# Kernel optimization log

Hardware: AMD Instinct MI355X
Metric: run time of the kernel (lower is better)

The kernel has to match this reference:

```python
import jax, jax.numpy as jnp
import numpy as np

PSIZE = 3
PSTRIDE = 3
N = PSIZE * PSTRIDE   # 9 attention tokens
P = PSIZE ** 2        # 9 pixels per token


def setup_inputs() -> dict:
    key = jax.random.key(0)
    k1, k2, k3, k4, k5 = jax.random.split(key, 5)
    B, H, W, C = 8192, 9, 9, 256
    hidden = C // 2
    x = jax.random.normal(k1, (B, H, W, C), dtype=jnp.float32)
    W_fc = jax.random.normal(k2, (hidden, C), dtype=jnp.float32) * (C ** -0.5)
    b_fc = jax.random.normal(k3, (hidden,), dtype=jnp.float32) * 0.01
    block_idx = jax.random.randint(k4, (B,), 0, 1024, dtype=jnp.int32)
    match_vec = jax.random.randint(k5, (1024, 1), 0, 2, dtype=jnp.int32)
    return {"x": x, "W_fc": W_fc, "b_fc": b_fc, "block_idx": block_idx, "match_vec": match_vec}


def reference(x, W_fc, b_fc, block_idx, match_vec):
    B, H, Wd, C = x.shape
    hidden = W_fc.shape[0]
    scale = (hidden * P) ** -0.5

    # [B, pstride, psize, pstride, psize, C] -> patch-major [B, ps, ps, p, p, C]
    xv = x.reshape(B, PSTRIDE, PSIZE, PSTRIDE, PSIZE, C).transpose(0, 1, 3, 2, 4, 5)
    x_fc = xv.reshape(B, N, P, C)

    # linear projection C -> hidden, then flatten pixels: q [B, N, P*hidden]
    q = (jnp.einsum('bnpc,hc->bnph', x_fc, W_fc) + b_fc).reshape(B, N, P * hidden)

    attn = jnp.einsum('bnd,bmd->bnm', q, q) * scale  # [B, N, N]

    # additive mask: -100 on diagonal, zeroed out entirely for matched samples
    base = jnp.where(jnp.eye(N, dtype=bool), jnp.float32(-100.0), jnp.float32(0.0))
    cur_match = match_vec[block_idx].squeeze(-1)  # [B]
    mask = jnp.where(cur_match[:, None, None] == 1, jnp.float32(0.0), base[None])

    attn = jax.nn.softmax(attn + mask, axis=-1)

    v = xv.reshape(B, N, P * C)
    out = attn @ v  # [B, N, P*C]

    out = out.reshape(B, PSTRIDE, PSTRIDE, PSIZE, PSIZE, C)
    out = out.transpose(0, 1, 3, 2, 4, 5).reshape(B, H, Wd, C)
    return out
```

## Files before the change

kernel.cpp:

```cpp
#include <hip/hip_runtime.h>

typedef short short8 __attribute__((ext_vector_type(8)));
typedef float floatx16 __attribute__((ext_vector_type(16)));
typedef float floatx4 __attribute__((ext_vector_type(4)));

#define ROWS 81
#define CDIM 256
#define XT   0
#define QT   41472
#define SC   66048
#define AB   70144
#define TOT  70656

#define SWX(r) ((((r) & 15) << 4) ^ (((r) & 8) << 3))

__device__ __forceinline__ unsigned short f2bf(float f) {
    union { float f; unsigned int u; } v; v.f = f;
    return (unsigned short)((v.u + 0x7FFFu + ((v.u >> 16) & 1u)) >> 16);
}

__device__ __forceinline__ unsigned int cvtpk(float lo, float hi) {
    unsigned int r;
    asm("v_cvt_pk_bf16_f32 %0, %1, %2" : "=v"(r) : "v"(lo), "v"(hi));
    return r;
}

__global__ void wconv_kernel(const float* __restrict__ W,
                             unsigned short* __restrict__ Wb, int n) {
    int i = blockIdx.x * 256 + threadIdx.x;
    if (i < n) Wb[i] = f2bf(W[i]);
}

__device__ __forceinline__ void stage_store(char* smem, int k, float4 a0, float4 a1) {
    int gr = k >> 5;
    int c0 = (k & 31) * 8;
    int hh = gr / 9, ww = gr - hh * 9;
    int p = (hh % 3) * 3 + (ww % 3);
    int m = (hh / 3) * 3 + (ww / 3);
    int r = p * 9 + m;
    uint4 v;
    v.x = cvtpk(a0.x, a0.y);
    v.y = cvtpk(a0.z, a0.w);
    v.z = cvtpk(a1.x, a1.y);
    v.w = cvtpk(a1.z, a1.w);
    *(uint4*)(smem + XT + r * 512 + ((c0 * 2) ^ SWX(r))) = v;
}

__global__ __launch_bounds__(512, 2)
void attn_kernel(const float* __restrict__ x,
                 const unsigned short* __restrict__ Wb,
                 const float* __restrict__ b_fc,
                 const int* __restrict__ block_idx,
                 const int* __restrict__ match_vec,
                 float* __restrict__ out)
{
    __shared__ __align__(16) char smem[TOT];
    const int b     = blockIdx.x;
    const int t     = threadIdx.x;
    const int lane  = t & 63;
    const int wave  = t >> 6;
    const int l15   = lane & 15;
    const int kg    = lane >> 4;
    const int l31   = lane & 31;
    const int khalf = lane >> 5;

    int cm = 0;
    if (t < 9) cm = match_vec[block_idx[b]];

    const int rh = (wave & 1) * 48;
    const int hg = (wave >> 1) * 32;

    short8 wfrag[2][8];
#pragma unroll
    for (int s2 = 0; s2 < 2; ++s2) {
        const unsigned short* wr = Wb + (hg + s2 * 16 + l15) * CDIM + kg * 8;
#pragma unroll
        for (int ks = 0; ks < 8; ++ks)
            wfrag[s2][ks] = *(const short8*)(wr + ks * 32);
    }
    float bias2[2];
    bias2[0] = b_fc[hg + l15];
    bias2[1] = b_fc[hg + 16 + l15];

    {
        const float* xb = x + (size_t)b * (ROWS * CDIM);
        float4 a0[5], a1[5], t0, t1;
#pragma unroll
        for (int j = 0; j < 5; ++j) {
            int k = t + 512 * j;
            a0[j] = *(const float4*)(xb + k * 8);
            a1[j] = *(const float4*)(xb + k * 8 + 4);
        }
        const bool tail = (t < 32);
        if (tail) {
            t0 = *(const float4*)(xb + (2560 + t) * 8);
            t1 = *(const float4*)(xb + (2560 + t) * 8 + 4);
        }
#pragma unroll
        for (int j = 0; j < 5; ++j) stage_store(smem, t + 512 * j, a0[j], a1[j]);
        if (tail) stage_store(smem, 2560 + t, t0, t1);
    }
    __syncthreads();

    {
        floatx4 acc[3][2];
#pragma unroll
        for (int ii = 0; ii < 3; ++ii)
#pragma unroll
            for (int s2 = 0; s2 < 2; ++s2)
#pragma unroll
                for (int j = 0; j < 4; ++j) acc[ii][s2][j] = 0.f;
#pragma unroll
        for (int ks = 0; ks < 8; ++ks) {
            int cb = ks * 64 + kg * 16;
#pragma unroll
            for (int tile = 0; tile < 3; ++tile) {
                int r = rh + tile * 16 + l15;
                short8 a = *(const short8*)(smem + XT + r * 512 + (cb ^ SWX(r)));
                acc[tile][0] = __builtin_amdgcn_mfma_f32_16x16x32_bf16(a, wfrag[0][ks], acc[tile][0], 0, 0, 0);
                acc[tile][1] = __builtin_amdgcn_mfma_f32_16x16x32_bf16(a, wfrag[1][ks], acc[tile][1], 0, 0, 0);
            }
        }
#pragma unroll
        for (int tile = 0; tile < 3; ++tile)
#pragma unroll
            for (int s2 = 0; s2 < 2; ++s2) {
                int h2 = (hg + s2 * 16 + l15) * 2;
#pragma unroll
                for (int reg = 0; reg < 4; ++reg) {
                    int r = rh + tile * 16 + kg * 4 + reg;
                    *(unsigned short*)(smem + QT + r * 256 + (h2 ^ ((r & 15) << 4))) =
                        f2bf(acc[tile][s2][reg] + bias2[s2]);
                }
            }
    }
    __syncthreads();

    if (wave < 4) {
        floatx4 g;
#pragma unroll
        for (int ii = 0; ii < 4; ++ii) g[ii] = 0.f;
        int nc = (l15 < 9) ? l15 : 8;
#pragma unroll
        for (int s = 0; s < 9; ++s) {
            int ks = wave + s * 4;
            int kk = ks * 32 + kg * 8;
            int p  = kk >> 7;
            int h0 = (kk & 127) * 2;
            int row = p * 9 + nc;
            short8 f = *(const short8*)(smem + QT + row * 256 + (h0 ^ ((row & 15) << 4)));
            g = __builtin_amdgcn_mfma_f32_16x16x32_bf16(f, f, g, 0, 0, 0);
        }
        float* sc = (float*)(smem + SC + wave * 1024);
#pragma unroll
        for (int reg = 0; reg < 4; ++reg)
            sc[(kg * 4 + reg) * 16 + l15] = g[reg];
    }
    __syncthreads();

    if (t < 9) {
        const float scale = 0.029462782549439483f;
        const float* sc0 = (const float*)(smem + SC);
        const float* sc1 = (const float*)(smem + SC + 1024);
        const float* sc2 = (const float*)(smem + SC + 2048);
        const float* sc3 = (const float*)(smem + SC + 3072);
        float s[9];
        float mx = -1e30f;
#pragma unroll
        for (int m = 0; m < 9; ++m) {
            int o = t * 16 + m;
            float v = (sc0[o] + sc1[o] + sc2[o] + sc3[o]) * scale;
            if (m == t && cm != 1) v -= 100.f;
            s[m] = v;
            mx = fmaxf(mx, v);
        }
        float sum = 0.f;
#pragma unroll
        for (int m = 0; m < 9; ++m) { s[m] = __expf(s[m] - mx); sum += s[m]; }
        float inv = 1.f / sum;
        unsigned short* ab = (unsigned short*)(smem + AB) + t * 16;
#pragma unroll
        for (int m = 0; m < 9; ++m) ab[m] = f2bf(s[m] * inv);
#pragma unroll
        for (int m = 9; m < 16; ++m) ab[m] = 0;
    }
    __syncthreads();

    {
        const int n  = l31;
        const int nm = (n < 9) ? n : 0;
        short8 bf = *(const short8*)(smem + AB + nm * 32 + khalf * 16);
        floatx16 zero16;
#pragma unroll
        for (int ii = 0; ii < 16; ++ii) zero16[ii] = 0.f;
        float* ob = out + (size_t)b * (ROWS * CDIM);
        int hh = 0, ww = 0;
        if (n < 9) { hh = (n / 3) * 3; ww = (n % 3) * 3; }
#pragma unroll
        for (int tt = 0; tt < 9; ++tt) {
            int tile = wave * 9 + tt;
            int p = tile >> 3;
            int c = (tile & 7) * 32 + l31;
            short8 af;
#pragma unroll
            for (int j = 0; j < 8; ++j) {
                int mm = khalf * 8 + j; if (mm > 8) mm = 8;
                int row = p * 9 + mm;
                af[j] = *(const short*)(smem + XT + row * 512 + ((c * 2) ^ SWX(row)));
            }
            floatx16 dacc = __builtin_amdgcn_mfma_f32_32x32x16_bf16(af, bf, zero16, 0, 0, 0);
            if (n < 9) {
#pragma unroll
                for (int q2 = 0; q2 < 4; ++q2) {
                    int c0 = (tile & 7) * 32 + q2 * 8 + khalf * 4;
                    int gr = (hh + p / 3) * 9 + (ww + p % 3);
                    *(float4*)(ob + gr * CDIM + c0) =
                        make_float4(dacc[q2 * 4 + 0], dacc[q2 * 4 + 1],
                                    dacc[q2 * 4 + 2], dacc[q2 * 4 + 3]);
                }
            }
        }
    }
}

extern "C" void kernel_launch(void* const* d_in, const int* in_sizes, int n_in,
                              void* d_out, int out_size, void* d_ws, size_t ws_size,
                              hipStream_t stream) {
    const float* x    = (const float*)d_in[0];
    const float* W    = (const float*)d_in[1];
    const float* bfc  = (const float*)d_in[2];
    const int*   bidx = (const int*)d_in[3];
    const int*   mvec = (const int*)d_in[4];
    float* outp = (float*)d_out;
    unsigned short* Wb = (unsigned short*)d_ws;

    int nW = in_sizes[1];
    wconv_kernel<<<(nW + 255) / 256, 256, 0, stream>>>(W, Wb, nW);

    int B = in_sizes[0] / (ROWS * CDIM);
    attn_kernel<<<B, 512, 0, stream>>>(x, Wb, bfc, bidx, mvec, outp);
}
```

Before: 345.5 us.

## Make attention kernel persistent with double-buffered prefetch of next batch's input

The kernel becomes persistent: a grid of at most 256 blocks each loops over a contiguous chunk of batch elements. The x tile is double-buffered in shared memory. Wave 0 computes the Gram matrix and the softmax alone, while the other seven waves load and convert the next batch element into the spare buffer. This hides global load latency behind compute and removes a barrier and the cross-wave score reduction, but raises LDS use to about 109KB per block, which limits occupancy to one block per CU. Only 256 blocks may also underfill the device's CUs.

```diff
diff --git a/kernel.cpp b/kernel.cpp
--- a/kernel.cpp
+++ b/kernel.cpp
@@ -6,11 +6,11 @@
 
 #define ROWS 81
 #define CDIM 256
-#define XT   0
-#define QT   41472
-#define SC   66048
-#define AB   70144
-#define TOT  70656
+#define XSZ  41472
+#define QT   82944
+#define SC   107520
+#define AB   108544
+#define TOT  109056
 
 #define SWX(r) ((((r) & 15) << 4) ^ (((r) & 8) << 3))
 
@@ -31,7 +31,7 @@
     if (i < n) Wb[i] = f2bf(W[i]);
 }
 
-__device__ __forceinline__ void stage_store(char* smem, int k, float4 a0, float4 a1) {
+__device__ __forceinline__ void stage_store(char* xbuf, int k, float4 a0, float4 a1) {
     int gr = k >> 5;
     int c0 = (k & 31) * 8;
     int hh = gr / 9, ww = gr - hh * 9;
@@ -43,7 +43,7 @@
     v.y = cvtpk(a0.z, a0.w);
     v.z = cvtpk(a1.x, a1.y);
     v.w = cvtpk(a1.z, a1.w);
-    *(uint4*)(smem + XT + r * 512 + ((c0 * 2) ^ SWX(r))) = v;
+    *(uint4*)(xbuf + r * 512 + ((c0 * 2) ^ SWX(r))) = v;
 }
 
 __global__ __launch_bounds__(512, 2)
@@ -52,10 +52,10 @@
                  const float* __restrict__ b_fc,
                  const int* __restrict__ block_idx,
                  const int* __restrict__ match_vec,
-                 float* __restrict__ out)
+                 float* __restrict__ out,
+                 int B, int nIter)
 {
     __shared__ __align__(16) char smem[TOT];
-    const int b     = blockIdx.x;
     const int t     = threadIdx.x;
     const int lane  = t & 63;
     const int wave  = t >> 6;
@@ -63,9 +63,8 @@
     const int kg    = lane >> 4;
     const int l31   = lane & 31;
     const int khalf = lane >> 5;
-
-    int cm = 0;
-    if (t < 9) cm = match_vec[block_idx[b]];
+    const int base  = blockIdx.x * nIter;
+    if (base >= B) return;
 
     const int rh = (wave & 1) * 48;
     const int hg = (wave >> 1) * 32;
@@ -83,7 +82,7 @@
     bias2[1] = b_fc[hg + 16 + l15];
 
     {
-        const float* xb = x + (size_t)b * (ROWS * CDIM);
+        const float* xb = x + (size_t)base * (ROWS * CDIM);
         float4 a0[5], a1[5], t0, t1;
 #pragma unroll
         for (int j = 0; j < 5; ++j) {
@@ -102,121 +101,147 @@
     }
     __syncthreads();
 
-    {
-        floatx4 acc[3][2];
-#pragma unroll
-        for (int ii = 0; ii < 3; ++ii)
-#pragma unroll
-            for (int s2 = 0; s2 < 2; ++s2)
-#pragma unroll
-                for (int j = 0; j < 4; ++j) acc[ii][s2][j] = 0.f;
-#pragma unroll
-        for (int ks = 0; ks < 8; ++ks) {
-            int cb = ks * 64 + kg * 16;
-#pragma unroll
-            for (int tile = 0; tile < 3; ++tile) {
-                int r = rh + tile * 16 + l15;
-                short8 a = *(const short8*)(smem + XT + r * 512 + (cb ^ SWX(r)));
-                acc[tile][0] = __builtin_amdgcn_mfma_f32_16x16x32_bf16(a, wfrag[0][ks], acc[tile][0], 0, 0, 0);
-                acc[tile][1] = __builtin_amdgcn_mfma_f32_16x16x32_bf16(a, wfrag[1][ks], acc[tile][1], 0, 0, 0);
-            }
-        }
-#pragma unroll
-        for (int tile = 0; tile < 3; ++tile)
-#pragma unroll
-            for (int s2 = 0; s2 < 2; ++s2) {
-                int h2 = (hg + s2 * 16 + l15) * 2;
-#pragma unroll
-                for (int reg = 0; reg < 4; ++reg) {
-                    int r = rh + tile * 16 + kg * 4 + reg;
-                    *(unsigned short*)(smem + QT + r * 256 + (h2 ^ ((r & 15) << 4))) =
-                        f2bf(acc[tile][s2][reg] + bias2[s2]);
-                }
-            }
-    }
-    __syncthreads();
-
-    if (wave < 4) {
-        floatx4 g;
-#pragma unroll
-        for (int ii = 0; ii < 4; ++ii) g[ii] = 0.f;
-        int nc = (l15 < 9) ? l15 : 8;
-#pragma unroll
-        for (int s = 0; s < 9; ++s) {
-            int ks = wave + s * 4;
-            int kk = ks * 32 + kg * 8;
-            int p  = kk >> 7;
-            int h0 = (kk & 127) * 2;
-            int row = p * 9 + nc;
-            short8 f = *(const short8*)(smem + QT + row * 256 + (h0 ^ ((row & 15) << 4)));
-            g = __builtin_amdgcn_mfma_f32_16x16x32_bf16(f, f, g, 0, 0, 0);
-        }
-        float* sc = (float*)(smem + SC + wave * 1024);
-#pragma unroll
-        for (int reg = 0; reg < 4; ++reg)
-            sc[(kg * 4 + reg) * 16 + l15] = g[reg];
-    }
-    __syncthreads();
-
-    if (t < 9) {
-        const float scale = 0.029462782549439483f;
-        const float* sc0 = (const float*)(smem + SC);
-        const float* sc1 = (const float*)(smem + SC + 1024);
-        const float* sc2 = (const float*)(smem + SC + 2048);
-        const float* sc3 = (const float*)(smem + SC + 3072);
-        float s[9];
-        float mx = -1e30f;
-#pragma unroll
-        for (int m = 0; m < 9; ++m) {
-            int o = t * 16 + m;
-            float v = (sc0[o] + sc1[o] + sc2[o] + sc3[o]) * scale;
-            if (m == t && cm != 1) v -= 100.f;
-            s[m] = v;
-            mx = fmaxf(mx, v);
-        }
-        float sum = 0.f;
-#pragma unroll
-        for (int m = 0; m < 9; ++m) { s[m] = __expf(s[m] - mx); sum += s[m]; }
-        float inv = 1.f / sum;
-        unsigned short* ab = (unsigned short*)(smem + AB) + t * 16;
-#pragma unroll
-        for (int m = 0; m < 9; ++m) ab[m] = f2bf(s[m] * inv);
-#pragma unroll
-        for (int m = 9; m < 16; ++m) ab[m] = 0;
-    }
-    __syncthreads();
-
-    {
-        const int n  = l31;
-        const int nm = (n < 9) ? n : 0;
-        short8 bf = *(const short8*)(smem + AB + nm * 32 + khalf * 16);
-        floatx16 zero16;
-#pragma unroll
-        for (int ii = 0; ii < 16; ++ii) zero16[ii] = 0.f;
-        float* ob = out + (size_t)b * (ROWS * CDIM);
-        int hh = 0, ww = 0;
-        if (n < 9) { hh = (n / 3) * 3; ww = (n % 3) * 3; }
-#pragma unroll
-        for (int tt = 0; tt < 9; ++tt) {
-            int tile = wave * 9 + tt;
-            int p = tile >> 3;
-            int c = (tile & 7) * 32 + l31;
-            short8 af;
-#pragma unroll
-            for (int j = 0; j < 8; ++j) {
-                int mm = khalf * 8 + j; if (mm > 8) mm = 8;
-                int row = p * 9 + mm;
-                af[j] = *(const short*)(smem + XT + row * 512 + ((c * 2) ^ SWX(row)));
-            }
-            floatx16 dacc = __builtin_amdgcn_mfma_f32_32x32x16_bf16(af, bf, zero16, 0, 0, 0);
-            if (n < 9) {
-#pragma unroll
-                for (int q2 = 0; q2 < 4; ++q2) {
-                    int c0 = (tile & 7) * 32 + q2 * 8 + khalf * 4;
-                    int gr = (hh + p / 3) * 9 + (ww + p % 3);
-                    *(float4*)(ob + gr * CDIM + c0) =
-                        make_float4(dacc[q2 * 4 + 0], dacc[q2 * 4 + 1],
-                                    dacc[q2 * 4 + 2], dacc[q2 * 4 + 3]);
+    for (int it = 0; it < nIter && base + it < B; ++it) {
+        const int b = base + it;
+        char* xc = smem + (it & 1) * XSZ;
+        char* xn = smem + ((it & 1) ^ 1) * XSZ;
+        const bool hasNext = (it + 1 < nIter) && (b + 1 < B);
+
+        int cm = 0;
+        if (t < 9) cm = match_vec[block_idx[b]];
+
+        {
+            floatx4 acc[3][2];
+#pragma unroll
+            for (int ii = 0; ii < 3; ++ii)
+#pragma unroll
+                for (int s2 = 0; s2 < 2; ++s2)
+#pragma unroll
+                    for (int j = 0; j < 4; ++j) acc[ii][s2][j] = 0.f;
+#pragma unroll
+            for (int ks = 0; ks < 8; ++ks) {
+                int cb = ks * 64 + kg * 16;
+#pragma unroll
+                for (int tile = 0; tile < 3; ++tile) {
+                    int r = rh + tile * 16 + l15;
+                    short8 a = *(const short8*)(xc + r * 512 + (cb ^ SWX(r)));
+                    acc[tile][0] = __builtin_amdgcn_mfma_f32_16x16x32_bf16(a, wfrag[0][ks], acc[tile][0], 0, 0, 0);
+                    acc[tile][1] = __builtin_amdgcn_mfma_f32_16x16x32_bf16(a, wfrag[1][ks], acc[tile][1], 0, 0, 0);
+                }
+            }
+#pragma unroll
+            for (int tile = 0; tile < 3; ++tile)
+#pragma unroll
+                for (int s2 = 0; s2 < 2; ++s2) {
+                    int h2 = (hg + s2 * 16 + l15) * 2;
+#pragma unroll
+                    for (int reg = 0; reg < 4; ++reg) {
+                        int r = rh + tile * 16 + kg * 4 + reg;
+                        *(unsigned short*)(smem + QT + r * 256 + (h2 ^ ((r & 15) << 4))) =
+                            f2bf(acc[tile][s2][reg] + bias2[s2]);
+                    }
+                }
+        }
+        __syncthreads();
+
+        if (wave == 0) {
+            floatx4 s0, s1, s2, s3;
+#pragma unroll
+            for (int ii = 0; ii < 4; ++ii) { s0[ii] = 0.f; s1[ii] = 0.f; s2[ii] = 0.f; s3[ii] = 0.f; }
+            int nc = (l15 < 9) ? l15 : 8;
+#pragma unroll
+            for (int s = 0; s < 9; ++s) {
+#pragma unroll
+                for (int ii = 0; ii < 4; ++ii) {
+                    int ks = ii + s * 4;
+                    int kk = ks * 32 + kg * 8;
+                    int p  = kk >> 7;
+                    int h0 = (kk & 127) * 2;
+                    int row = p * 9 + nc;
+                    short8 f = *(const short8*)(smem + QT + row * 256 + (h0 ^ ((row & 15) << 4)));
+                    floatx4 tmp = __builtin_amdgcn_mfma_f32_16x16x32_bf16(
+                        f, f, (ii == 0 ? s0 : ii == 1 ? s1 : ii == 2 ? s2 : s3), 0, 0, 0);
+                    if (ii == 0) s0 = tmp; else if (ii == 1) s1 = tmp; else if (ii == 2) s2 = tmp; else s3 = tmp;
+                }
+            }
+            float* sc = (float*)(smem + SC);
+#pragma unroll
+            for (int reg = 0; reg < 4; ++reg)
+                sc[(kg * 4 + reg) * 16 + l15] = s0[reg] + s1[reg] + s2[reg] + s3[reg];
+
+            if (lane < 9) {
+                const float scale = 0.029462782549439483f;
+                float s[9];
+                float mx = -1e30f;
+#pragma unroll
+                for (int m = 0; m < 9; ++m) {
+                    float v = sc[lane * 16 + m] * scale;
+                    if (m == lane && cm != 1) v -= 100.f;
+                    s[m] = v;
+                    mx = fmaxf(mx, v);
+                }
+                float sum = 0.f;
+#pragma unroll
+                for (int m = 0; m < 9; ++m) { s[m] = __expf(s[m] - mx); sum += s[m]; }
+                float inv = 1.f / sum;
+                unsigned short* ab = (unsigned short*)(smem + AB) + lane * 16;
+#pragma unroll
+                for (int m = 0; m < 9; ++m) ab[m] = f2bf(s[m] * inv);
+#pragma unroll
+                for (int m = 9; m < 16; ++m) ab[m] = 0;
+            }
+        } else if (hasNext) {
+            const int ts = t - 64;
+            const float* xg = x + (size_t)(b + 1) * (ROWS * CDIM);
+            float4 a0[6], a1[6];
+#pragma unroll
+            for (int j = 0; j < 6; ++j) {
+                int k = ts + 448 * j;
+                if (k < ROWS * 32) {
+                    a0[j] = *(const float4*)(xg + k * 8);
+                    a1[j] = *(const float4*)(xg + k * 8 + 4);
+                }
+            }
+#pragma unroll
+            for (int j = 0; j < 6; ++j) {
+                int k = ts + 448 * j;
+                if (k < ROWS * 32) stage_store(xn, k, a0[j], a1[j]);
+            }
+        }
+        __syncthreads();
+
+        {
+            const int n  = l31;
+            const int nm = (n < 9) ? n : 0;
+            short8 bf = *(const short8*)(smem + AB + nm * 32 + khalf * 16);
+            floatx16 zero16;
+#pragma unroll
+            for (int ii = 0; ii < 16; ++ii) zero16[ii] = 0.f;
+            float* ob = out + (size_t)b * (ROWS * CDIM);
+            int hh = 0, ww = 0;
+            if (n < 9) { hh = (n / 3) * 3; ww = (n % 3) * 3; }
+#pragma unroll
+            for (int tt = 0; tt < 9; ++tt) {
+                int tile = wave * 9 + tt;
+                int p = tile >> 3;
+                int c = (tile & 7) * 32 + l31;
+                short8 af;
+#pragma unroll
+                for (int j = 0; j < 8; ++j) {
+                    int mm = khalf * 8 + j; if (mm > 8) mm = 8;
+                    int row = p * 9 + mm;
+                    af[j] = *(const short*)(xc + row * 512 + ((c * 2) ^ SWX(row)));
+                }
+                floatx16 dacc = __builtin_amdgcn_mfma_f32_32x32x16_bf16(af, bf, zero16, 0, 0, 0);
+                if (n < 9) {
+#pragma unroll
+                    for (int q2 = 0; q2 < 4; ++q2) {
+                        int c0 = (tile & 7) * 32 + q2 * 8 + khalf * 4;
+                        int gr = (hh + p / 3) * 9 + (ww + p % 3);
+                        *(float4*)(ob + gr * CDIM + c0) =
+                            make_float4(dacc[q2 * 4 + 0], dacc[q2 * 4 + 1],
+                                        dacc[q2 * 4 + 2], dacc[q2 * 4 + 3]);
+                    }
                 }
             }
         }
@@ -238,5 +263,7 @@
     wconv_kernel<<<(nW + 255) / 256, 256, 0, stream>>>(W, Wb, nW);
 
     int B = in_sizes[0] / (ROWS * CDIM);
-    attn_kernel<<<B, 512, 0, stream>>>(x, Wb, bfc, bidx, mvec, outp);
-}
+    int grid = (B < 256) ? B : 256;
+    int nIter = (B + grid - 1) / grid;
+    attn_kernel<<<grid, 512, 0, stream>>>(x, Wb, bfc, bidx, mvec, outp, B, nIter);
+}
```

After: 772.1 us. 123% more time.
